# Performance work log

Hardware: AMD Instinct MI355X
Metric: run time of the kernel (lower is better)

The kernel has to match this reference:

```python
import jax, jax.numpy as jnp
import numpy as np

B, N, C = 8, 2048, 1024
SPARSITY = 0.8
K_KEEP = int(N * SPARSITY)  # 1638
NEG = 1e10


def setup_inputs() -> dict:
    key = jax.random.key(0)
    ks = jax.random.split(key, 7)
    s = 1.0 / np.sqrt(C)
    return {
        "x": jax.random.normal(ks[0], (B, N, C), dtype=jnp.float32),
        "Wq": jax.random.uniform(ks[1], (C, C), dtype=jnp.float32, minval=-s, maxval=s),
        "bq": jax.random.uniform(ks[2], (C,), dtype=jnp.float32, minval=-s, maxval=s),
        "Wk": jax.random.uniform(ks[3], (C, C), dtype=jnp.float32, minval=-s, maxval=s),
        "bk": jax.random.uniform(ks[4], (C,), dtype=jnp.float32, minval=-s, maxval=s),
        "Wv": jax.random.uniform(ks[5], (C, C), dtype=jnp.float32, minval=-s, maxval=s),
        "bv": jax.random.uniform(ks[6], (C,), dtype=jnp.float32, minval=-s, maxval=s),
    }


def reference(x, Wq, bq, Wk, bk, Wv, bv):
    # Linear projections (torch Linear: y = x @ W.T + b)
    Q = jnp.einsum("bnc,dc->bnd", x, Wq) + bq
    Kt = jnp.einsum("bnc,dc->bnd", x, Wk) + bk
    V = jnp.einsum("bnc,dc->bnd", x, Wv) + bv
    attn = jnp.einsum("bnd,bmd->bnm", Q, Kt) / jnp.sqrt(jnp.float32(C))  # [B,N,N]
    _, idx = jax.lax.top_k(attn, K_KEEP)  # idx: [B,N,K_KEEP]
    bI = jnp.arange(B)[:, None, None]
    nI = jnp.arange(N)[None, :, None]
    mask = jnp.zeros_like(attn).at[bI, nI, idx].set(1.0)
    attn = attn * mask - NEG * (1.0 - mask)
    attn = jax.nn.softmax(attn, axis=-1)
    return jnp.einsum("bnm,bmd->bnd", attn, V)
```

## Files before the change

### kernel.cpp

```cpp
#include <hip/hip_runtime.h>

typedef _Float16 f16;
typedef __attribute__((ext_vector_type(8))) _Float16 f16x8;
typedef __attribute__((ext_vector_type(4))) _Float16 f16x4;
typedef __attribute__((ext_vector_type(4))) float f32x4;

constexpr int BB = 8;
constexpr int NN = 2048;
constexpr int CC = 1024;
constexpr int MTOT = BB * NN;
constexpr int KKEEP = 1638;

__device__ __forceinline__ void gl_lds16(const void* g, void* l) {
  __builtin_amdgcn_global_load_lds((__attribute__((address_space(1))) void*)g,
                                   (__attribute__((address_space(3))) void*)l,
                                   16, 0, 0);
}

__global__ __launch_bounds__(256) void cvt_f32_f16(const float* __restrict__ s,
                                                   f16* __restrict__ d, int n4) {
  int i = blockIdx.x * 256 + threadIdx.x;
  if (i < n4) {
    float4 f = ((const float4*)s)[i];
    f16x4 o = {(f16)f.x, (f16)f.y, (f16)f.z, (f16)f.w};
    ((f16x4*)d)[i] = o;
  }
}

template <int MODE>
__global__ __launch_bounds__(256, 2) void gemm_bt(
    const f16* __restrict__ A, const f16* __restrict__ B,
    const float* __restrict__ bias, void* __restrict__ Cout,
    int K, int lda, int ldb, int ldc, float scale, int ldct,
    long strideA, long strideB, long strideC) {
  const f16* Ab = A + (size_t)blockIdx.z * strideA;
  const f16* Bbp = B + (size_t)blockIdx.z * strideB;

  const int bm = blockIdx.x * 128;
  const int bn = blockIdx.y * 128;
  const int tid = threadIdx.x;
  const int wave = tid >> 6;
  const int lane = tid & 63;
  const int wy = wave >> 1, wx = wave & 1;

  __shared__ f16 As[128 * 32];
  __shared__ f16 Bs[128 * 32];

  f32x4 acc[4][4];
#pragma unroll
  for (int i = 0; i < 4; i++)
#pragma unroll
    for (int j = 0; j < 4; j++) acc[i][j] = (f32x4){0.f, 0.f, 0.f, 0.f};

  const int sr = wave * 32 + (lane >> 2);
  const int sc = (lane & 3) * 8;
  const f16* gA0 = Ab + (size_t)(bm + sr) * lda + sc;
  const f16* gA1 = gA0 + (size_t)16 * lda;
  const f16* gB0 = Bbp + (size_t)(bn + sr) * ldb + sc;
  const f16* gB1 = gB0 + (size_t)16 * ldb;
  f16* lA0 = As + (wave * 32) * 32;
  f16* lA1 = As + (wave * 32 + 16) * 32;
  f16* lB0 = Bs + (wave * 32) * 32;
  f16* lB1 = Bs + (wave * 32 + 16) * 32;

  const int frm = wy * 64 + (lane & 15);
  const int frn = wx * 64 + (lane & 15);
  const int kq = (lane >> 4) * 8;

  for (int k0 = 0; k0 < K; k0 += 32) {
    gl_lds16(gA0 + k0, lA0);
    gl_lds16(gA1 + k0, lA1);
    gl_lds16(gB0 + k0, lB0);
    gl_lds16(gB1 + k0, lB1);
    __syncthreads();
    f16x8 av[4], bv[4];
#pragma unroll
    for (int i = 0; i < 4; i++)
      av[i] = *(const f16x8*)(As + (frm + 16 * i) * 32 + kq);
#pragma unroll
    for (int i = 0; i < 4; i++)
      bv[i] = *(const f16x8*)(Bs + (frn + 16 * i) * 32 + kq);
#pragma unroll
    for (int i = 0; i < 4; i++)
#pragma unroll
      for (int j = 0; j < 4; j++)
        acc[i][j] =
            __builtin_amdgcn_mfma_f32_16x16x32_f16(av[i], bv[j], acc[i][j], 0, 0, 0);
    __syncthreads();
  }

  const int q = lane >> 4;
  const int ci = lane & 15;
#pragma unroll
  for (int i = 0; i < 4; i++) {
#pragma unroll
    for (int j = 0; j < 4; j++) {
      const int row0 = bm + wy * 64 + i * 16 + q * 4;
      const int col = bn + wx * 64 + j * 16 + ci;
      if (MODE == 0) {
        float* C = (float*)Cout + (size_t)blockIdx.z * strideC;
#pragma unroll
        for (int r = 0; r < 4; r++)
          C[(size_t)(row0 + r) * ldc + col] = acc[i][j][r] * scale;
      } else if (MODE == 1) {
        f16* C = (f16*)Cout + (size_t)blockIdx.z * strideC;
        const float bb = bias[col];
#pragma unroll
        for (int r = 0; r < 4; r++)
          C[(size_t)(row0 + r) * ldc + col] = (f16)(acc[i][j][r] + bb);
      } else {
        f16* C = (f16*)Cout;
        const float bb = bias[col];
        f16x4 o;
#pragma unroll
        for (int r = 0; r < 4; r++) o[r] = (f16)(acc[i][j][r] + bb);
        *(f16x4*)(C + (size_t)col * ldct + row0) = o;
      }
    }
  }
}

__global__ __launch_bounds__(256) void topk_softmax_kernel(float* __restrict__ S) {
  const size_t row = blockIdx.x;
  float* srow = S + row * 2048;
  f16* prow = (f16*)srow;
  const int t = threadIdx.x;
  const int lane = t & 63;
  const int wave = t >> 6;

  float v[8];
  float4 f0 = ((const float4*)srow)[2 * t];
  float4 f1 = ((const float4*)srow)[2 * t + 1];
  v[0] = f0.x; v[1] = f0.y; v[2] = f0.z; v[3] = f0.w;
  v[4] = f1.x; v[5] = f1.y; v[6] = f1.z; v[7] = f1.w;

  unsigned u[8];
#pragma unroll
  for (int j = 0; j < 8; j++) {
    unsigned b = __float_as_uint(v[j]);
    u[j] = (b & 0x80000000u) ? ~b : (b | 0x80000000u);
  }

  __shared__ int hist4[256 * 4];
  __shared__ int wagg[4];
  __shared__ float wf[4];
  __shared__ unsigned sh_thr;
  __shared__ int sh_want;

  unsigned prefix = 0;
  int want = KKEEP;
  for (int shift = 24; shift >= 0; shift -= 8) {
    ((int4*)hist4)[t] = (int4){0, 0, 0, 0};
    __syncthreads();
#pragma unroll
    for (int j = 0; j < 8; j++) {
      bool cand = (shift == 24) || ((u[j] >> (shift + 8)) == (prefix >> (shift + 8)));
      if (cand) atomicAdd(&hist4[(((u[j] >> shift) & 255) << 2) + wave], 1);
    }
    __syncthreads();
    int4 hh = ((const int4*)hist4)[t];
    int h = hh.x + hh.y + hh.z + hh.w;
    int sfx = h;
#pragma unroll
    for (int off = 1; off < 64; off <<= 1) {
      int o = __shfl_down(sfx, off, 64);
      sfx += (lane + off < 64) ? o : 0;
    }
    if (lane == 0) wagg[wave] = sfx;
    __syncthreads();
    int hi = 0;
#pragma unroll
    for (int w = 0; w < 4; w++) hi += (w > wave) ? wagg[w] : 0;
    const int cum = sfx + hi;
    const int above = cum - h;
    if (cum >= want && above < want) {
      sh_thr = prefix | ((unsigned)t << shift);
      sh_want = want - above;
    }
    __syncthreads();
    prefix = sh_thr;
    want = sh_want;
  }

  int eqf[8];
  int ceq = 0;
#pragma unroll
  for (int j = 0; j < 8; j++) {
    eqf[j] = (u[j] == prefix) ? 1 : 0;
    ceq += eqf[j];
  }
  int inc = ceq;
#pragma unroll
  for (int off = 1; off < 64; off <<= 1) {
    int o = __shfl_up(inc, off, 64);
    inc += (lane >= off) ? o : 0;
  }
  if (lane == 63) wagg[wave] = inc;
  __syncthreads();
  int pre = 0;
#pragma unroll
  for (int w = 0; w < 4; w++) pre += (w < wave) ? wagg[w] : 0;
  const int excl = pre + inc - ceq;

  float mx = v[0];
#pragma unroll
  for (int j = 1; j < 8; j++) mx = fmaxf(mx, v[j]);
#pragma unroll
  for (int off = 32; off > 0; off >>= 1) mx = fmaxf(mx, __shfl_xor(mx, off, 64));
  if (lane == 0) wf[wave] = mx;
  __syncthreads();
  mx = fmaxf(fmaxf(wf[0], wf[1]), fmaxf(wf[2], wf[3]));
  __syncthreads();

  float e[8];
  float lsum = 0.f;
  int r = excl;
#pragma unroll
  for (int j = 0; j < 8; j++) {
    bool kept;
    if (u[j] > prefix) {
      kept = true;
    } else if (eqf[j]) {
      kept = (r < want);
      r++;
    } else {
      kept = false;
    }
    e[j] = kept ? __expf(v[j] - mx) : 0.f;
    lsum += e[j];
  }
#pragma unroll
  for (int off = 32; off > 0; off >>= 1) lsum += __shfl_xor(lsum, off, 64);
  if (lane == 0) wf[wave] = lsum;
  __syncthreads();
  const float inv = 1.0f / (wf[0] + wf[1] + wf[2] + wf[3]);

  f16x8 o;
#pragma unroll
  for (int j = 0; j < 8; j++) o[j] = (f16)(e[j] * inv);
  *(f16x8*)(prow + t * 8) = o;
}

extern "C" void kernel_launch(void* const* d_in, const int* in_sizes, int n_in,
                              void* d_out, int out_size, void* d_ws, size_t ws_size,
                              hipStream_t stream) {
  (void)in_sizes; (void)n_in; (void)out_size; (void)ws_size;
  const float* x = (const float*)d_in[0];
  const float* Wq = (const float*)d_in[1];
  const float* bq = (const float*)d_in[2];
  const float* Wk = (const float*)d_in[3];
  const float* bk = (const float*)d_in[4];
  const float* Wv = (const float*)d_in[5];
  const float* bv = (const float*)d_in[6];
  float* out = (float*)d_out;

  char* ws = (char*)d_ws;
  f16* qb = (f16*)(ws + 0);
  f16* kb = (f16*)(ws + 33554432);
  f16* vtb = (f16*)(ws + 67108864);
  float* S = (float*)(ws + 100663296);
  f16* xb = (f16*)(ws + 100663296);
  f16* wqb = (f16*)(ws + 134217728);
  f16* wkb = (f16*)(ws + 136314880);
  f16* wvb = (f16*)(ws + 138412032);

  cvt_f32_f16<<<(MTOT * CC / 4 + 255) / 256, 256, 0, stream>>>(x, xb, MTOT * CC / 4);
  cvt_f32_f16<<<(CC * CC / 4 + 255) / 256, 256, 0, stream>>>(Wq, wqb, CC * CC / 4);
  cvt_f32_f16<<<(CC * CC / 4 + 255) / 256, 256, 0, stream>>>(Wk, wkb, CC * CC / 4);
  cvt_f32_f16<<<(CC * CC / 4 + 255) / 256, 256, 0, stream>>>(Wv, wvb, CC * CC / 4);

  gemm_bt<1><<<dim3(MTOT / 128, CC / 128, 1), 256, 0, stream>>>(
      xb, wqb, bq, qb, CC, CC, CC, CC, 1.f, 0, 0, 0, 0);
  gemm_bt<1><<<dim3(MTOT / 128, CC / 128, 1), 256, 0, stream>>>(
      xb, wkb, bk, kb, CC, CC, CC, CC, 1.f, 0, 0, 0, 0);
  gemm_bt<2><<<dim3(MTOT / 128, CC / 128, 1), 256, 0, stream>>>(
      xb, wvb, bv, vtb, CC, CC, CC, 0, 1.f, MTOT, 0, 0, 0);

  gemm_bt<0><<<dim3(NN / 128, NN / 128, BB), 256, 0, stream>>>(
      qb, kb, nullptr, S, CC, CC, CC, NN, 1.f / 32.f, 0,
      (long)NN * CC, (long)NN * CC, (long)NN * NN);

  topk_softmax_kernel<<<MTOT, 256, 0, stream>>>(S);

  gemm_bt<0><<<dim3(NN / 128, CC / 128, BB), 256, 0, stream>>>(
      (const f16*)S, vtb, nullptr, out, NN, 2 * NN, MTOT, CC, 1.f, 0,
      (long)NN * 2 * NN, (long)NN, (long)NN * CC);
}
```

Before: 534.9 us.

## Replace multi-pass radix top-k with single-pass quantized histogram select

The four-pass 8-bit radix select in the top-k softmax kernel becomes a single 2048-bin histogram over each row's min-max range. Ties in the threshold bin are settled by ranking against at most 128 candidates stored in LDS. The row max from the min/max reduction is reused for the softmax, which drops a separate reduction and several barriers. Probabilities now go to a dense f16 buffer with leading dimension N instead of being packed inside the fp32 score rows, so the final GEMM reads contiguous rows. The risk is wrong results if more than 128 values land in the threshold bin.

```diff
diff --git a/kernel.cpp b/kernel.cpp
--- a/kernel.cpp
+++ b/kernel.cpp
@@ -120,10 +120,11 @@
   }
 }
 
-__global__ __launch_bounds__(256) void topk_softmax_kernel(float* __restrict__ S) {
+__global__ __launch_bounds__(256) void topk_softmax_kernel(
+    const float* __restrict__ S, f16* __restrict__ P) {
   const size_t row = blockIdx.x;
-  float* srow = S + row * 2048;
-  f16* prow = (f16*)srow;
+  const float* srow = S + row * 2048;
+  f16* prow = P + row * 2048;
   const int t = threadIdx.x;
   const int lane = t & 63;
   const int wave = t >> 6;
@@ -134,99 +135,113 @@
   v[0] = f0.x; v[1] = f0.y; v[2] = f0.z; v[3] = f0.w;
   v[4] = f1.x; v[5] = f1.y; v[6] = f1.z; v[7] = f1.w;
 
-  unsigned u[8];
+  __shared__ float wlo[4], whi[4];
+  __shared__ float wf[4];
+  __shared__ int wagg[4];
+  __shared__ int hist[2048];
+  __shared__ float cval[128];
+  __shared__ int cidx[128];
+  __shared__ int cnum;
+  __shared__ int sh_thr, sh_want;
+
+  float lo = v[0], hi = v[0];
+#pragma unroll
+  for (int j = 1; j < 8; j++) { lo = fminf(lo, v[j]); hi = fmaxf(hi, v[j]); }
+#pragma unroll
+  for (int off = 32; off > 0; off >>= 1) {
+    lo = fminf(lo, __shfl_xor(lo, off, 64));
+    hi = fmaxf(hi, __shfl_xor(hi, off, 64));
+  }
+  if (lane == 0) { wlo[wave] = lo; whi[wave] = hi; }
+  if (t == 0) cnum = 0;
+  ((int4*)hist)[2 * t] = (int4){0, 0, 0, 0};
+  ((int4*)hist)[2 * t + 1] = (int4){0, 0, 0, 0};
+  __syncthreads();
+  lo = fminf(fminf(wlo[0], wlo[1]), fminf(wlo[2], wlo[3]));
+  hi = fmaxf(fmaxf(whi[0], whi[1]), fmaxf(whi[2], whi[3]));
+
+  if (hi == lo) {
+    const float w = 1.0f / (float)KKEEP;
+    f16x8 o;
+#pragma unroll
+    for (int j = 0; j < 8; j++) o[j] = (f16)((t * 8 + j < KKEEP) ? w : 0.f);
+    *(f16x8*)(prow + t * 8) = o;
+    return;
+  }
+
+  const float qs = 2048.0f / (hi - lo);
+  int key[8];
 #pragma unroll
   for (int j = 0; j < 8; j++) {
-    unsigned b = __float_as_uint(v[j]);
-    u[j] = (b & 0x80000000u) ? ~b : (b | 0x80000000u);
-  }
-
-  __shared__ int hist4[256 * 4];
-  __shared__ int wagg[4];
-  __shared__ float wf[4];
-  __shared__ unsigned sh_thr;
-  __shared__ int sh_want;
-
-  unsigned prefix = 0;
-  int want = KKEEP;
-  for (int shift = 24; shift >= 0; shift -= 8) {
-    ((int4*)hist4)[t] = (int4){0, 0, 0, 0};
-    __syncthreads();
-#pragma unroll
-    for (int j = 0; j < 8; j++) {
-      bool cand = (shift == 24) || ((u[j] >> (shift + 8)) == (prefix >> (shift + 8)));
-      if (cand) atomicAdd(&hist4[(((u[j] >> shift) & 255) << 2) + wave], 1);
+    int k = (int)((v[j] - lo) * qs);
+    key[j] = (k > 2047) ? 2047 : k;
+  }
+#pragma unroll
+  for (int j = 0; j < 8; j++) atomicAdd(&hist[key[j]], 1);
+  __syncthreads();
+
+  int4 h0 = ((const int4*)hist)[2 * t];
+  int4 h1 = ((const int4*)hist)[2 * t + 1];
+  int h[8] = {h0.x, h0.y, h0.z, h0.w, h1.x, h1.y, h1.z, h1.w};
+  int s[8];
+  s[7] = h[7];
+#pragma unroll
+  for (int j = 6; j >= 0; j--) s[j] = s[j + 1] + h[j];
+  const int partial = s[0];
+  int sfx = partial;
+#pragma unroll
+  for (int off = 1; off < 64; off <<= 1) {
+    int o = __shfl_down(sfx, off, 64);
+    sfx += (lane + off < 64) ? o : 0;
+  }
+  if (lane == 0) wagg[wave] = sfx;
+  __syncthreads();
+  int hiw = 0;
+#pragma unroll
+  for (int w = 0; w < 4; w++) hiw += (w > wave) ? wagg[w] : 0;
+  const int base = (sfx - partial) + hiw;
+#pragma unroll
+  for (int j = 0; j < 8; j++) {
+    const int cum = s[j] + base;
+    const int above = cum - h[j];
+    if (cum >= KKEEP && above < KKEEP) {
+      sh_thr = 8 * t + j;
+      sh_want = KKEEP - above;
     }
-    __syncthreads();
-    int4 hh = ((const int4*)hist4)[t];
-    int h = hh.x + hh.y + hh.z + hh.w;
-    int sfx = h;
-#pragma unroll
-    for (int off = 1; off < 64; off <<= 1) {
-      int o = __shfl_down(sfx, off, 64);
-      sfx += (lane + off < 64) ? o : 0;
+  }
+  __syncthreads();
+  const int thr = sh_thr;
+  const int wantin = sh_want;
+
+#pragma unroll
+  for (int j = 0; j < 8; j++) {
+    if (key[j] == thr) {
+      int slot = atomicAdd(&cnum, 1);
+      if (slot < 128) { cval[slot] = v[j]; cidx[slot] = t * 8 + j; }
     }
-    if (lane == 0) wagg[wave] = sfx;
-    __syncthreads();
-    int hi = 0;
-#pragma unroll
-    for (int w = 0; w < 4; w++) hi += (w > wave) ? wagg[w] : 0;
-    const int cum = sfx + hi;
-    const int above = cum - h;
-    if (cum >= want && above < want) {
-      sh_thr = prefix | ((unsigned)t << shift);
-      sh_want = want - above;
-    }
-    __syncthreads();
-    prefix = sh_thr;
-    want = sh_want;
-  }
-
-  int eqf[8];
-  int ceq = 0;
-#pragma unroll
-  for (int j = 0; j < 8; j++) {
-    eqf[j] = (u[j] == prefix) ? 1 : 0;
-    ceq += eqf[j];
-  }
-  int inc = ceq;
-#pragma unroll
-  for (int off = 1; off < 64; off <<= 1) {
-    int o = __shfl_up(inc, off, 64);
-    inc += (lane >= off) ? o : 0;
-  }
-  if (lane == 63) wagg[wave] = inc;
-  __syncthreads();
-  int pre = 0;
-#pragma unroll
-  for (int w = 0; w < 4; w++) pre += (w < wave) ? wagg[w] : 0;
-  const int excl = pre + inc - ceq;
-
-  float mx = v[0];
-#pragma unroll
-  for (int j = 1; j < 8; j++) mx = fmaxf(mx, v[j]);
-#pragma unroll
-  for (int off = 32; off > 0; off >>= 1) mx = fmaxf(mx, __shfl_xor(mx, off, 64));
-  if (lane == 0) wf[wave] = mx;
-  __syncthreads();
-  mx = fmaxf(fmaxf(wf[0], wf[1]), fmaxf(wf[2], wf[3]));
-  __syncthreads();
+  }
+  __syncthreads();
+  const int n = (cnum < 128) ? cnum : 128;
 
   float e[8];
   float lsum = 0.f;
-  int r = excl;
 #pragma unroll
   for (int j = 0; j < 8; j++) {
     bool kept;
-    if (u[j] > prefix) {
+    if (key[j] > thr) {
       kept = true;
-    } else if (eqf[j]) {
-      kept = (r < want);
-      r++;
+    } else if (key[j] < thr) {
+      kept = false;
     } else {
-      kept = false;
+      const int myidx = t * 8 + j;
+      int rank = 0;
+      for (int c = 0; c < n; c++) {
+        const float cv = cval[c];
+        rank += (cv > v[j] || (cv == v[j] && cidx[c] < myidx)) ? 1 : 0;
+      }
+      kept = rank < wantin;
     }
-    e[j] = kept ? __expf(v[j] - mx) : 0.f;
+    e[j] = kept ? __expf(v[j] - hi) : 0.f;
     lsum += e[j];
   }
 #pragma unroll
@@ -263,6 +278,7 @@
   f16* wqb = (f16*)(ws + 134217728);
   f16* wkb = (f16*)(ws + 136314880);
   f16* wvb = (f16*)(ws + 138412032);
+  f16* Pc = (f16*)(ws + 0);
 
   cvt_f32_f16<<<(MTOT * CC / 4 + 255) / 256, 256, 0, stream>>>(x, xb, MTOT * CC / 4);
   cvt_f32_f16<<<(CC * CC / 4 + 255) / 256, 256, 0, stream>>>(Wq, wqb, CC * CC / 4);
@@ -280,9 +296,9 @@
       qb, kb, nullptr, S, CC, CC, CC, NN, 1.f / 32.f, 0,
       (long)NN * CC, (long)NN * CC, (long)NN * NN);
 
-  topk_softmax_kernel<<<MTOT, 256, 0, stream>>>(S);
+  topk_softmax_kernel<<<MTOT, 256, 0, stream>>>(S, Pc);
 
   gemm_bt<0><<<dim3(NN / 128, CC / 128, BB), 256, 0, stream>>>(
-      (const f16*)S, vtb, nullptr, out, NN, 2 * NN, MTOT, CC, 1.f, 0,
-      (long)NN * 2 * NN, (long)NN, (long)NN * CC);
-}
+      Pc, vtb, nullptr, out, NN, NN, MTOT, CC, 1.f, 0,
+      (long)NN * NN, (long)NN, (long)NN * CC);
+}
```

After: 484.0 us. 9.5% less time.
